# Kernel optimization log

Hardware: AMD Instinct MI355X
Metric: run time of the kernel (lower is better)

The kernel has to match this reference:

```python
import jax, jax.numpy as jnp
import numpy as np

B, N, D = 8, 2048, 8        # batch, nodes, input_dim == hidden_dim
E, DEC = 8, 128             # embedding_dim, decoder_dim


def _leaky(x, slope):
    return jnp.where(x >= 0, x, slope * x)


def _sage(x, attn, inv_deg, w, b):
    # adj transposed on dims (1,2) then left-matmul: new[b,i,d] = sum_j attn[b,j,i] x[b,j,d]
    new_x = jnp.einsum('bji,bjd->bid', attn, x)
    new_x = jnp.matmul(inv_deg, new_x)
    new_x = jnp.matmul(new_x, w)
    self_x = jnp.matmul(x, b)
    c = jnp.concatenate([new_x, self_x], axis=2)
    norm = jnp.sqrt(jnp.sum(c * c, axis=2, keepdims=True))
    return c / jnp.maximum(norm, 1e-12)  # F.normalize(p=2, dim=2)


def setup_inputs():
    key = jax.random.key(0)
    ks = jax.random.split(key, 12)
    x = jax.random.normal(ks[0], (B, N, D), jnp.float32)
    adj = jax.random.randint(ks[1], (B, N, N), 0, 2).astype(jnp.int32)
    deg = jnp.sum(adj.astype(jnp.float32), axis=2)
    inv_deg = jax.vmap(jnp.diag)(1.0 / (deg + 1.0))  # [B,N,N] diagonal
    g = np.sqrt(2.0)  # xavier-style scale stand-in
    W = jax.random.normal(ks[2], (D, D), jnp.float32) * (g / np.sqrt(2 * D))
    a = jax.random.normal(ks[3], (2 * D, 1), jnp.float32) * (g / np.sqrt(2 * D + 1))
    w1 = jax.random.normal(ks[4], (D, D), jnp.float32) * 0.3
    b1 = jax.random.normal(ks[5], (D, D), jnp.float32) * 0.3
    w2 = jax.random.normal(ks[6], (2 * D, D), jnp.float32) * 0.3
    b2 = jax.random.normal(ks[7], (2 * D, D), jnp.float32) * 0.3
    w3 = jax.random.normal(ks[8], (2 * D, E), jnp.float32) * 0.3
    b3 = jax.random.normal(ks[9], (2 * D, E), jnp.float32) * 0.3
    P1 = jax.random.normal(ks[10], (2 * E, DEC), jnp.float32) * 0.1
    P2 = jax.random.normal(ks[11], (DEC, DEC), jnp.float32) * 0.1
    return {"x": x, "adj": adj, "inv_deg": inv_deg, "W": W, "a": a,
            "w1": w1, "b1": b1, "w2": w2, "b2": b2, "w3": w3, "b3": b3,
            "P1": P1, "P2": P2}


def reference(x, adj, inv_deg, W, a, w1, b1, w2, b2, w3, b3, P1, P2):
    h = jnp.matmul(x, W)                          # [B,N,D]
    # e[b,i,j] = leaky(h[b,i].a1 + h[b,j].a2), equivalent to cat+matmul without O(N^2*2D) tensor
    f1 = jnp.matmul(h, a[:D, 0])                  # [B,N]
    f2 = jnp.matmul(h, a[D:, 0])                  # [B,N]
    e = _leaky(f1[:, :, None] + f2[:, None, :], 0.2)
    e = jnp.where(adj > 0, e, jnp.float32(-9e15))
    attn = jax.nn.softmax(e, axis=2)              # [B,N,N]
    out = _leaky(_sage(x, attn, inv_deg, w1, b1), 0.1)
    out = _leaky(_sage(out, attn, inv_deg, w2, b2), 0.1)
    out = _leaky(_sage(out, attn, inv_deg, w3, b3), 0.1)
    da = out[:, N - 2]                            # [B,2E]
    db = out[:, N - 1]
    ypred = jnp.einsum('bi,id,de,je,bj->b', da, P1, P2, P1, db)
    return ypred[:, None]
```

## Files before the change

kernel.cpp:

```cpp
#include <hip/hip_runtime.h>
#include <math.h>

constexpr int CB   = 8;
constexpr int CN   = 2048;
constexpr int CD   = 8;
constexpr int CDEC = 128;
constexpr int CBN  = CB * CN;
constexpr int NWRD = CN / 64;
constexpr int JSP  = 32;
constexpr int JLEN = CN / JSP;

__device__ __forceinline__ float msel(unsigned long long m, int lane, float p) {
  return ((m >> lane) & 1ull) ? p : 0.f;
}

__global__ void prep_k(const float* __restrict__ x,
                       const float* __restrict__ W, const float* __restrict__ a,
                       float4* __restrict__ pk, float4* __restrict__ qk) {
  int t = blockIdx.x * blockDim.x + threadIdx.x;
  if (t >= CBN) return;
  const float* xr = x + (size_t)t * CD;
  float h[CD];
#pragma unroll
  for (int d = 0; d < CD; ++d) {
    float s = 0.f;
#pragma unroll
    for (int k = 0; k < CD; ++k) s = fmaf(xr[k], W[k * CD + d], s);
    h[d] = s;
  }
  float s1 = 0.f, s2 = 0.f;
#pragma unroll
  for (int d = 0; d < CD; ++d) { s1 = fmaf(h[d], a[d], s1); s2 = fmaf(h[d], a[CD + d], s2); }
  pk[t] = make_float4(s1, expf(s1), expf(0.2f * s1), 0.f);
  qk[t] = make_float4(s2, expf(s2), expf(0.2f * s2), 0.f);
}

__global__ __launch_bounds__(256) void mask_k(const int* __restrict__ adj,
    float4* __restrict__ pk, const float4* __restrict__ qk,
    unsigned long long* __restrict__ maskT) {
  const int lane = threadIdx.x & 63;
  const int gw2 = blockIdx.x * 4 + (threadIdx.x >> 6);
  const int b = gw2 >> 9;
  const int jw = gw2 & 511;
  const int* ab = adj + (size_t)b * CN * CN;
  const float4* qb = qk + (size_t)b * CN;
  float f1[4];
#pragma unroll
  for (int r = 0; r < 4; ++r) f1[r] = pk[b * CN + jw + 512 * r].x;
  float A[4] = {0.f, 0.f, 0.f, 0.f}, C[4] = {0.f, 0.f, 0.f, 0.f};
  int deg[4] = {0, 0, 0, 0};
  for (int k = 0; k < NWRD; ++k) {
    int i = k * 64 + lane;
    float4 q = qb[i];
    unsigned long long m[4];
#pragma unroll
    for (int r = 0; r < 4; ++r) {
      bool bit = ab[(size_t)(jw + 512 * r) * CN + i] > 0;
      m[r] = __ballot(bit);
      bool cond = (f1[r] + q.x) >= 0.f;
      A[r] += (bit && cond) ? q.y : 0.f;
      C[r] += (bit && !cond) ? q.z : 0.f;
    }
    if (lane == 0) {
#pragma unroll
      for (int r = 0; r < 4; ++r) {
        maskT[((size_t)(b * NWRD + k)) * CN + jw + 512 * r] = m[r];
        deg[r] += __popcll(m[r]);
      }
    }
  }
#pragma unroll
  for (int r = 0; r < 4; ++r) {
#pragma unroll
    for (int off = 32; off; off >>= 1) {
      A[r] += __shfl_down(A[r], off);
      C[r] += __shfl_down(C[r], off);
    }
  }
  if (lane == 0) {
#pragma unroll
    for (int r = 0; r < 4; ++r) {
      int gr = b * CN + jw + 512 * r;
      float4 pj = pk[gr];
      float s = pj.y * A[r] + pj.z * C[r];
      float ga = (s > 0.f) ? pj.y / s : 0.f;
      float gb = (s > 0.f) ? pj.z / s : 0.f;
      float dv = 1.f / (float)(deg[r] + 1);
      pk[gr] = make_float4(pj.x, ga, gb, dv);
    }
  }
}

template <int DIN>
__global__ __launch_bounds__(256) void agg_k(const float* __restrict__ feat,
                      const unsigned long long* __restrict__ maskT,
                      const float4* __restrict__ pk, const float4* __restrict__ qk,
                      const float* __restrict__ wmat, float* __restrict__ part) {
  const int js = blockIdx.x, ic = blockIdx.y, b = blockIdx.z;
  const int t = threadIdx.x;
  const int w = __builtin_amdgcn_readfirstlane(t >> 6);
  const int lane = t & 63;
  const int i1 = ic * 512 + t, i2 = i1 + 256;
  const int gi1 = b * CN + i1, gi2 = b * CN + i2;
  float4 q1 = qk[gi1], q2 = qk[gi2];
  const unsigned long long* mc1 = maskT + ((size_t)(b * NWRD + ic * 8 + w)) * CN + js * JLEN;
  const unsigned long long* mc2 = maskT + ((size_t)(b * NWRD + ic * 8 + 4 + w)) * CN + js * JLEN;
  const float4* pb = pk + (size_t)b * CN + js * JLEN;
  const float* fb  = feat + ((size_t)b * CN + js * JLEN) * DIN;
  float acc1[DIN], acc2[DIN];
#pragma unroll
  for (int d = 0; d < DIN; ++d) { acc1[d] = 0.f; acc2[d] = 0.f; }
#pragma unroll 4
  for (int jj = 0; jj < JLEN; ++jj) {
    unsigned long long m1 = mc1[jj];
    unsigned long long m2 = mc2[jj];
    float4 pj = pb[jj];
    const float* fr = fb + jj * DIN;
    float wA = msel(m1, lane, fmaxf(pj.y * q1.y, pj.z * q1.z));
    float wB = msel(m2, lane, fmaxf(pj.y * q2.y, pj.z * q2.z));
#pragma unroll
    for (int d = 0; d < DIN; ++d) {
      acc1[d] = fmaf(wA, fr[d], acc1[d]);
      acc2[d] = fmaf(wB, fr[d], acc2[d]);
    }
  }
  float o1[8], o2[8];
#pragma unroll
  for (int o = 0; o < 8; ++o) {
    float s1 = 0.f, s2 = 0.f;
#pragma unroll
    for (int d = 0; d < DIN; ++d) {
      s1 = fmaf(acc1[d], wmat[d * 8 + o], s1);
      s2 = fmaf(acc2[d], wmat[d * 8 + o], s2);
    }
    o1[o] = s1;
    o2[o] = s2;
  }
  float4* p1 = (float4*)(part + ((size_t)js * CBN + gi1) * 8);
  float4* p2 = (float4*)(part + ((size_t)js * CBN + gi2) * 8);
  p1[0] = make_float4(o1[0], o1[1], o1[2], o1[3]);
  p1[1] = make_float4(o1[4], o1[5], o1[6], o1[7]);
  p2[0] = make_float4(o2[0], o2[1], o2[2], o2[3]);
  p2[1] = make_float4(o2[4], o2[5], o2[6], o2[7]);
}

__global__ void epi8_k(const float* __restrict__ part, const float* __restrict__ feat,
                       const float4* __restrict__ pk, const float* __restrict__ bmat,
                       float* __restrict__ out) {
  int t = blockIdx.x * blockDim.x + threadIdx.x;
  if (t >= CBN) return;
  float4 a0 = make_float4(0.f, 0.f, 0.f, 0.f), a1 = a0;
  for (int p_ = 0; p_ < JSP; ++p_) {
    const float4* pr = (const float4*)(part + ((size_t)p_ * CBN + t) * 8);
    float4 r0 = pr[0], r1 = pr[1];
    a0.x += r0.x; a0.y += r0.y; a0.z += r0.z; a0.w += r0.w;
    a1.x += r1.x; a1.y += r1.y; a1.z += r1.z; a1.w += r1.w;
  }
  float ag[8] = {a0.x, a0.y, a0.z, a0.w, a1.x, a1.y, a1.z, a1.w};
  float di = pk[t].w;
  const float* fr = feat + (size_t)t * 8;
  float c[16];
#pragma unroll
  for (int o = 0; o < 8; ++o) {
    float s2 = 0.f;
#pragma unroll
    for (int d = 0; d < 8; ++d) s2 = fmaf(fr[d], bmat[d * 8 + o], s2);
    c[o] = ag[o] * di;
    c[8 + o] = s2;
  }
  float nn = 0.f;
#pragma unroll
  for (int k = 0; k < 16; ++k) nn += c[k] * c[k];
  float inv = 1.f / fmaxf(sqrtf(nn), 1e-12f);
  float4* orow = (float4*)(out + (size_t)t * 16);
#pragma unroll
  for (int q = 0; q < 4; ++q) {
    float v0 = c[q*4+0]*inv, v1 = c[q*4+1]*inv, v2 = c[q*4+2]*inv, v3 = c[q*4+3]*inv;
    orow[q] = make_float4(v0 >= 0.f ? v0 : 0.1f*v0, v1 >= 0.f ? v1 : 0.1f*v1,
                          v2 >= 0.f ? v2 : 0.1f*v2, v3 >= 0.f ? v3 : 0.1f*v3);
  }
}

__global__ __launch_bounds__(256) void epi16f_k(
    const float* __restrict__ out1, const float* __restrict__ part2,
    const unsigned long long* __restrict__ maskT,
    const float4* __restrict__ pk, const float4* __restrict__ qk,
    const float* __restrict__ b2,
    float* __restrict__ gpart, float* __restrict__ self2) {
  __shared__ float redA[4][16], redB[4][16];
  const int t = threadIdx.x;
  const int lane = t & 63, wv = t >> 6;
  const int gr = blockIdx.x * 256 + t;
  const int b = blockIdx.x >> 3, blk8 = blockIdx.x & 7;
  const int j = gr - b * CN;
  const int ia = CN - 2, ib = CN - 1;
  float ag[8] = {0.f,0.f,0.f,0.f,0.f,0.f,0.f,0.f};
  for (int p = 0; p < JSP; ++p) {
    const float4* pr = (const float4*)(part2 + ((size_t)p * CBN + gr) * 8);
    float4 r0 = pr[0], r1 = pr[1];
    ag[0] += r0.x; ag[1] += r0.y; ag[2] += r0.z; ag[3] += r0.w;
    ag[4] += r1.x; ag[5] += r1.y; ag[6] += r1.z; ag[7] += r1.w;
  }
  float4 pj = pk[gr];
  const float4* o1p = (const float4*)(out1 + (size_t)gr * 16);
  float4 g0 = o1p[0], g1 = o1p[1], g2 = o1p[2], g3 = o1p[3];
  float of[16] = {g0.x,g0.y,g0.z,g0.w, g1.x,g1.y,g1.z,g1.w,
                  g2.x,g2.y,g2.z,g2.w, g3.x,g3.y,g3.z,g3.w};
  float c[16];
#pragma unroll
  for (int o = 0; o < 8; ++o) {
    float s2 = 0.f;
#pragma unroll
    for (int d = 0; d < 16; ++d) s2 = fmaf(of[d], b2[d * 8 + o], s2);
    c[o] = ag[o] * pj.w;
    c[8 + o] = s2;
  }
  float nn = 0.f;
#pragma unroll
  for (int k = 0; k < 16; ++k) nn += c[k] * c[k];
  float inv = 1.f / fmaxf(sqrtf(nn), 1e-12f);
  float ff[16];
#pragma unroll
  for (int k = 0; k < 16; ++k) {
    float v = c[k] * inv;
    ff[k] = (v >= 0.f) ? v : 0.1f * v;
  }
  if (j == ia || j == ib) {
    float* s = self2 + ((size_t)b * 2 + (j == ib ? 1 : 0)) * 16;
#pragma unroll
    for (int d = 0; d < 16; ++d) s[d] = ff[d];
  }
  unsigned long long m = maskT[((size_t)(b * NWRD + (NWRD - 1))) * CN + j];
  float4 qa = qk[b * CN + ia], qb = qk[b * CN + ib];
  float wA = ((m >> 62) & 1ull) ? fmaxf(pj.y * qa.y, pj.z * qa.z) : 0.f;
  float wB = (m >> 63) ? fmaxf(pj.y * qb.y, pj.z * qb.z) : 0.f;
  float accA[16], accB[16];
#pragma unroll
  for (int d = 0; d < 16; ++d) { accA[d] = wA * ff[d]; accB[d] = wB * ff[d]; }
#pragma unroll
  for (int d = 0; d < 16; ++d) {
#pragma unroll
    for (int off = 32; off; off >>= 1) {
      accA[d] += __shfl_down(accA[d], off);
      accB[d] += __shfl_down(accB[d], off);
    }
  }
  if (lane == 0) {
#pragma unroll
    for (int d = 0; d < 16; ++d) { redA[wv][d] = accA[d]; redB[wv][d] = accB[d]; }
  }
  __syncthreads();
  if (t < 32) {
    int row = t >> 4, k = t & 15;
    float s = row ? (redB[0][k] + redB[1][k] + redB[2][k] + redB[3][k])
                  : (redA[0][k] + redA[1][k] + redA[2][k] + redA[3][k]);
    gpart[(((size_t)b * 8 + blk8) * 2 + row) * 16 + k] = s;
  }
}

__global__ __launch_bounds__(CDEC) void dec_k(
    const float* __restrict__ gpart, const float* __restrict__ self2,
    const float4* __restrict__ pk,
    const float* __restrict__ w3, const float* __restrict__ b3,
    const float* __restrict__ P1, const float* __restrict__ P2,
    float* __restrict__ y) {
  __shared__ float agA[16], agB[16], cA[16], cB[16], daF[16], dbF[16];
  __shared__ float vsh[CDEC], red[CDEC];
  const int b = blockIdx.x;
  const int t = threadIdx.x;
  const int ia = CN - 2, ib = CN - 1;
  if (t < 32) {
    int row = t >> 4, k = t & 15;
    float s = 0.f;
#pragma unroll
    for (int blk = 0; blk < 8; ++blk)
      s += gpart[(((size_t)b * 8 + blk) * 2 + row) * 16 + k];
    float dv = pk[b * CN + (row ? ib : ia)].w;
    (row ? agB : agA)[k] = s * dv;
  }
  __syncthreads();
  if (t < 32) {
    int row = t >> 4, k = t & 15;
    const float* ag = row ? agB : agA;
    const float* self = self2 + ((size_t)b * 2 + row) * 16;
    float s = 0.f;
    if (k < 8) {
#pragma unroll
      for (int d = 0; d < 16; ++d) s = fmaf(ag[d], w3[d * 8 + k], s);
    } else {
#pragma unroll
      for (int d = 0; d < 16; ++d) s = fmaf(self[d], b3[d * 8 + (k - 8)], s);
    }
    (row ? cB : cA)[k] = s;
  }
  __syncthreads();
  if (t < 32) {
    int row = t >> 4, k = t & 15;
    const float* c = row ? cB : cA;
    float nn = 0.f;
#pragma unroll
    for (int q = 0; q < 16; ++q) nn += c[q] * c[q];
    float inv = 1.f / fmaxf(sqrtf(nn), 1e-12f);
    float v = c[k] * inv;
    (row ? dbF : daF)[k] = (v >= 0.f) ? v : 0.1f * v;
  }
  __syncthreads();
  float ue = 0.f, ve = 0.f;
#pragma unroll
  for (int i = 0; i < 16; ++i) {
    ue = fmaf(daF[i], P1[i * CDEC + t], ue);
    ve = fmaf(dbF[i], P1[i * CDEC + t], ve);
  }
  vsh[t] = ve;
  __syncthreads();
  float s = 0.f;
  for (int e2 = 0; e2 < CDEC; ++e2) s = fmaf(P2[t * CDEC + e2], vsh[e2], s);
  red[t] = s * ue;
  __syncthreads();
  for (int off = 64; off; off >>= 1) {
    if (t < off) red[t] += red[t + off];
    __syncthreads();
  }
  if (t == 0) y[b] = red[0];
}

extern "C" void kernel_launch(void* const* d_in, const int* in_sizes, int n_in,
                              void* d_out, int out_size, void* d_ws, size_t ws_size,
                              hipStream_t stream) {
  const float* x  = (const float*)d_in[0];
  const int*   adj = (const int*)d_in[1];
  const float* W  = (const float*)d_in[3];
  const float* a  = (const float*)d_in[4];
  const float* w1 = (const float*)d_in[5];
  const float* b1 = (const float*)d_in[6];
  const float* w2 = (const float*)d_in[7];
  const float* b2 = (const float*)d_in[8];
  const float* w3 = (const float*)d_in[9];
  const float* b3 = (const float*)d_in[10];
  const float* P1 = (const float*)d_in[11];
  const float* P2 = (const float*)d_in[12];
  float* y = (float*)d_out;

  char* base = (char*)d_ws;
  size_t off = 0;
  auto alloc = [&](size_t bytes) -> void* {
    void* r = base + off;
    off += (bytes + 255) & ~(size_t)255;
    return r;
  };
  float4* pk = (float4*)alloc(sizeof(float4) * CBN);
  float4* qk = (float4*)alloc(sizeof(float4) * CBN);
  unsigned long long* maskT =
      (unsigned long long*)alloc(sizeof(unsigned long long) * (size_t)CBN * NWRD);
  float* out1  = (float*)alloc(sizeof(float) * (size_t)CBN * 16);
  float* part  = (float*)alloc(sizeof(float) * (size_t)JSP * CBN * 8);
  float* gpart = (float*)alloc(sizeof(float) * CB * 8 * 2 * 16);
  float* self2 = (float*)alloc(sizeof(float) * CB * 2 * 16);

  hipLaunchKernelGGL(prep_k, dim3(CBN / 256), dim3(256), 0, stream, x, W, a, pk, qk);
  hipLaunchKernelGGL(mask_k, dim3(1024), dim3(256), 0, stream, adj, pk, qk, maskT);
  hipLaunchKernelGGL(agg_k<8>, dim3(JSP, 4, CB), dim3(256), 0, stream, x, maskT, pk, qk, w1, part);
  hipLaunchKernelGGL(epi8_k, dim3(CBN / 256), dim3(256), 0, stream, part, x, pk, b1, out1);
  hipLaunchKernelGGL(agg_k<16>, dim3(JSP, 4, CB), dim3(256), 0, stream, out1, maskT, pk, qk, w2, part);
  hipLaunchKernelGGL(epi16f_k, dim3(CBN / 256), dim3(256), 0, stream,
                     out1, part, maskT, pk, qk, b2, gpart, self2);
  hipLaunchKernelGGL(dec_k, dim3(CB), dim3(CDEC), 0, stream,
                     gpart, self2, pk, w3, b3, P1, P2, y);
}
```

Baseline: 109.0 us.

## Apply layer weight matrices before aggregation to shrink layer-2 feature width

Uses associativity, attn^T (x W) = (attn^T x) W, to project node features through w and b before the attention aggregation rather than after. The second aggregation then reads 8-wide pre-projected features instead of the 16-wide layer-1 output, which halves its feature loads and inner FMAs. The self-term projections are computed in the producer kernels. This adds extra per-node buffers and a small dense matmul in prep and epi8, and slightly changes floating-point summation order.

```diff
diff --git a/kernel.cpp b/kernel.cpp
--- a/kernel.cpp
+++ b/kernel.cpp
@@ -16,7 +16,9 @@
 
 __global__ void prep_k(const float* __restrict__ x,
                        const float* __restrict__ W, const float* __restrict__ a,
-                       float4* __restrict__ pk, float4* __restrict__ qk) {
+                       const float* __restrict__ w1, const float* __restrict__ b1,
+                       float4* __restrict__ pk, float4* __restrict__ qk,
+                       float* __restrict__ feat1w, float* __restrict__ selfb1) {
   int t = blockIdx.x * blockDim.x + threadIdx.x;
   if (t >= CBN) return;
   const float* xr = x + (size_t)t * CD;
@@ -33,6 +35,23 @@
   for (int d = 0; d < CD; ++d) { s1 = fmaf(h[d], a[d], s1); s2 = fmaf(h[d], a[CD + d], s2); }
   pk[t] = make_float4(s1, expf(s1), expf(0.2f * s1), 0.f);
   qk[t] = make_float4(s2, expf(s2), expf(0.2f * s2), 0.f);
+  float fw[8], fb[8];
+#pragma unroll
+  for (int o = 0; o < 8; ++o) {
+    float sw = 0.f, sb = 0.f;
+#pragma unroll
+    for (int d = 0; d < CD; ++d) {
+      sw = fmaf(xr[d], w1[d * 8 + o], sw);
+      sb = fmaf(xr[d], b1[d * 8 + o], sb);
+    }
+    fw[o] = sw; fb[o] = sb;
+  }
+  float4* f4 = (float4*)(feat1w + (size_t)t * 8);
+  f4[0] = make_float4(fw[0], fw[1], fw[2], fw[3]);
+  f4[1] = make_float4(fw[4], fw[5], fw[6], fw[7]);
+  float4* s4 = (float4*)(selfb1 + (size_t)t * 8);
+  s4[0] = make_float4(fb[0], fb[1], fb[2], fb[3]);
+  s4[1] = make_float4(fb[4], fb[5], fb[6], fb[7]);
 }
 
 __global__ __launch_bounds__(256) void mask_k(const int* __restrict__ adj,
@@ -91,11 +110,10 @@
   }
 }
 
-template <int DIN>
-__global__ __launch_bounds__(256) void agg_k(const float* __restrict__ feat,
+__global__ __launch_bounds__(256) void aggf_k(const float* __restrict__ feat,
                       const unsigned long long* __restrict__ maskT,
                       const float4* __restrict__ pk, const float4* __restrict__ qk,
-                      const float* __restrict__ wmat, float* __restrict__ part) {
+                      float* __restrict__ part) {
   const int js = blockIdx.x, ic = blockIdx.y, b = blockIdx.z;
   const int t = threadIdx.x;
   const int w = __builtin_amdgcn_readfirstlane(t >> 6);
@@ -106,47 +124,36 @@
   const unsigned long long* mc1 = maskT + ((size_t)(b * NWRD + ic * 8 + w)) * CN + js * JLEN;
   const unsigned long long* mc2 = maskT + ((size_t)(b * NWRD + ic * 8 + 4 + w)) * CN + js * JLEN;
   const float4* pb = pk + (size_t)b * CN + js * JLEN;
-  const float* fb  = feat + ((size_t)b * CN + js * JLEN) * DIN;
-  float acc1[DIN], acc2[DIN];
-#pragma unroll
-  for (int d = 0; d < DIN; ++d) { acc1[d] = 0.f; acc2[d] = 0.f; }
+  const float* fb  = feat + ((size_t)b * CN + js * JLEN) * 8;
+  float acc1[8], acc2[8];
+#pragma unroll
+  for (int d = 0; d < 8; ++d) { acc1[d] = 0.f; acc2[d] = 0.f; }
 #pragma unroll 4
   for (int jj = 0; jj < JLEN; ++jj) {
     unsigned long long m1 = mc1[jj];
     unsigned long long m2 = mc2[jj];
     float4 pj = pb[jj];
-    const float* fr = fb + jj * DIN;
+    const float* fr = fb + jj * 8;
     float wA = msel(m1, lane, fmaxf(pj.y * q1.y, pj.z * q1.z));
     float wB = msel(m2, lane, fmaxf(pj.y * q2.y, pj.z * q2.z));
 #pragma unroll
-    for (int d = 0; d < DIN; ++d) {
+    for (int d = 0; d < 8; ++d) {
       acc1[d] = fmaf(wA, fr[d], acc1[d]);
       acc2[d] = fmaf(wB, fr[d], acc2[d]);
     }
   }
-  float o1[8], o2[8];
-#pragma unroll
-  for (int o = 0; o < 8; ++o) {
-    float s1 = 0.f, s2 = 0.f;
-#pragma unroll
-    for (int d = 0; d < DIN; ++d) {
-      s1 = fmaf(acc1[d], wmat[d * 8 + o], s1);
-      s2 = fmaf(acc2[d], wmat[d * 8 + o], s2);
-    }
-    o1[o] = s1;
-    o2[o] = s2;
-  }
   float4* p1 = (float4*)(part + ((size_t)js * CBN + gi1) * 8);
   float4* p2 = (float4*)(part + ((size_t)js * CBN + gi2) * 8);
-  p1[0] = make_float4(o1[0], o1[1], o1[2], o1[3]);
-  p1[1] = make_float4(o1[4], o1[5], o1[6], o1[7]);
-  p2[0] = make_float4(o2[0], o2[1], o2[2], o2[3]);
-  p2[1] = make_float4(o2[4], o2[5], o2[6], o2[7]);
-}
-
-__global__ void epi8_k(const float* __restrict__ part, const float* __restrict__ feat,
-                       const float4* __restrict__ pk, const float* __restrict__ bmat,
-                       float* __restrict__ out) {
+  p1[0] = make_float4(acc1[0], acc1[1], acc1[2], acc1[3]);
+  p1[1] = make_float4(acc1[4], acc1[5], acc1[6], acc1[7]);
+  p2[0] = make_float4(acc2[0], acc2[1], acc2[2], acc2[3]);
+  p2[1] = make_float4(acc2[4], acc2[5], acc2[6], acc2[7]);
+}
+
+__global__ void epi8_k(const float* __restrict__ part, const float* __restrict__ selfb1,
+                       const float4* __restrict__ pk,
+                       const float* __restrict__ w2, const float* __restrict__ b2,
+                       float* __restrict__ feat2w, float* __restrict__ selfb2) {
   int t = blockIdx.x * blockDim.x + threadIdx.x;
   if (t >= CBN) return;
   float4 a0 = make_float4(0.f, 0.f, 0.f, 0.f), a1 = a0;
@@ -156,36 +163,45 @@
     a0.x += r0.x; a0.y += r0.y; a0.z += r0.z; a0.w += r0.w;
     a1.x += r1.x; a1.y += r1.y; a1.z += r1.z; a1.w += r1.w;
   }
-  float ag[8] = {a0.x, a0.y, a0.z, a0.w, a1.x, a1.y, a1.z, a1.w};
   float di = pk[t].w;
-  const float* fr = feat + (size_t)t * 8;
-  float c[16];
-#pragma unroll
-  for (int o = 0; o < 8; ++o) {
-    float s2 = 0.f;
-#pragma unroll
-    for (int d = 0; d < 8; ++d) s2 = fmaf(fr[d], bmat[d * 8 + o], s2);
-    c[o] = ag[o] * di;
-    c[8 + o] = s2;
-  }
+  const float4* sb = (const float4*)(selfb1 + (size_t)t * 8);
+  float4 s0 = sb[0], s1 = sb[1];
+  float c[16] = {a0.x * di, a0.y * di, a0.z * di, a0.w * di,
+                 a1.x * di, a1.y * di, a1.z * di, a1.w * di,
+                 s0.x, s0.y, s0.z, s0.w, s1.x, s1.y, s1.z, s1.w};
   float nn = 0.f;
 #pragma unroll
   for (int k = 0; k < 16; ++k) nn += c[k] * c[k];
   float inv = 1.f / fmaxf(sqrtf(nn), 1e-12f);
-  float4* orow = (float4*)(out + (size_t)t * 16);
-#pragma unroll
-  for (int q = 0; q < 4; ++q) {
-    float v0 = c[q*4+0]*inv, v1 = c[q*4+1]*inv, v2 = c[q*4+2]*inv, v3 = c[q*4+3]*inv;
-    orow[q] = make_float4(v0 >= 0.f ? v0 : 0.1f*v0, v1 >= 0.f ? v1 : 0.1f*v1,
-                          v2 >= 0.f ? v2 : 0.1f*v2, v3 >= 0.f ? v3 : 0.1f*v3);
-  }
+  float ff[16];
+#pragma unroll
+  for (int k = 0; k < 16; ++k) {
+    float v = c[k] * inv;
+    ff[k] = (v >= 0.f) ? v : 0.1f * v;
+  }
+  float fw[8], fb[8];
+#pragma unroll
+  for (int o = 0; o < 8; ++o) {
+    float sw = 0.f, sb2_ = 0.f;
+#pragma unroll
+    for (int d = 0; d < 16; ++d) {
+      sw = fmaf(ff[d], w2[d * 8 + o], sw);
+      sb2_ = fmaf(ff[d], b2[d * 8 + o], sb2_);
+    }
+    fw[o] = sw; fb[o] = sb2_;
+  }
+  float4* f4 = (float4*)(feat2w + (size_t)t * 8);
+  f4[0] = make_float4(fw[0], fw[1], fw[2], fw[3]);
+  f4[1] = make_float4(fw[4], fw[5], fw[6], fw[7]);
+  float4* s4 = (float4*)(selfb2 + (size_t)t * 8);
+  s4[0] = make_float4(fb[0], fb[1], fb[2], fb[3]);
+  s4[1] = make_float4(fb[4], fb[5], fb[6], fb[7]);
 }
 
 __global__ __launch_bounds__(256) void epi16f_k(
-    const float* __restrict__ out1, const float* __restrict__ part2,
+    const float* __restrict__ part2, const float* __restrict__ selfb2,
     const unsigned long long* __restrict__ maskT,
     const float4* __restrict__ pk, const float4* __restrict__ qk,
-    const float* __restrict__ b2,
     float* __restrict__ gpart, float* __restrict__ self2) {
   __shared__ float redA[4][16], redB[4][16];
   const int t = threadIdx.x;
@@ -194,27 +210,19 @@
   const int b = blockIdx.x >> 3, blk8 = blockIdx.x & 7;
   const int j = gr - b * CN;
   const int ia = CN - 2, ib = CN - 1;
-  float ag[8] = {0.f,0.f,0.f,0.f,0.f,0.f,0.f,0.f};
+  float4 a0 = make_float4(0.f, 0.f, 0.f, 0.f), a1 = a0;
   for (int p = 0; p < JSP; ++p) {
     const float4* pr = (const float4*)(part2 + ((size_t)p * CBN + gr) * 8);
     float4 r0 = pr[0], r1 = pr[1];
-    ag[0] += r0.x; ag[1] += r0.y; ag[2] += r0.z; ag[3] += r0.w;
-    ag[4] += r1.x; ag[5] += r1.y; ag[6] += r1.z; ag[7] += r1.w;
+    a0.x += r0.x; a0.y += r0.y; a0.z += r0.z; a0.w += r0.w;
+    a1.x += r1.x; a1.y += r1.y; a1.z += r1.z; a1.w += r1.w;
   }
   float4 pj = pk[gr];
-  const float4* o1p = (const float4*)(out1 + (size_t)gr * 16);
-  float4 g0 = o1p[0], g1 = o1p[1], g2 = o1p[2], g3 = o1p[3];
-  float of[16] = {g0.x,g0.y,g0.z,g0.w, g1.x,g1.y,g1.z,g1.w,
-                  g2.x,g2.y,g2.z,g2.w, g3.x,g3.y,g3.z,g3.w};
-  float c[16];
-#pragma unroll
-  for (int o = 0; o < 8; ++o) {
-    float s2 = 0.f;
-#pragma unroll
-    for (int d = 0; d < 16; ++d) s2 = fmaf(of[d], b2[d * 8 + o], s2);
-    c[o] = ag[o] * pj.w;
-    c[8 + o] = s2;
-  }
+  const float4* sb = (const float4*)(selfb2 + (size_t)gr * 8);
+  float4 s0 = sb[0], s1 = sb[1];
+  float c[16] = {a0.x * pj.w, a0.y * pj.w, a0.z * pj.w, a0.w * pj.w,
+                 a1.x * pj.w, a1.y * pj.w, a1.z * pj.w, a1.w * pj.w,
+                 s0.x, s0.y, s0.z, s0.w, s1.x, s1.y, s1.z, s1.w};
   float nn = 0.f;
 #pragma unroll
   for (int k = 0; k < 16; ++k) nn += c[k] * c[k];
@@ -352,18 +360,23 @@
   float4* qk = (float4*)alloc(sizeof(float4) * CBN);
   unsigned long long* maskT =
       (unsigned long long*)alloc(sizeof(unsigned long long) * (size_t)CBN * NWRD);
-  float* out1  = (float*)alloc(sizeof(float) * (size_t)CBN * 16);
-  float* part  = (float*)alloc(sizeof(float) * (size_t)JSP * CBN * 8);
-  float* gpart = (float*)alloc(sizeof(float) * CB * 8 * 2 * 16);
-  float* self2 = (float*)alloc(sizeof(float) * CB * 2 * 16);
-
-  hipLaunchKernelGGL(prep_k, dim3(CBN / 256), dim3(256), 0, stream, x, W, a, pk, qk);
+  float* feat1w = (float*)alloc(sizeof(float) * (size_t)CBN * 8);
+  float* selfb1 = (float*)alloc(sizeof(float) * (size_t)CBN * 8);
+  float* feat2w = (float*)alloc(sizeof(float) * (size_t)CBN * 8);
+  float* selfb2 = (float*)alloc(sizeof(float) * (size_t)CBN * 8);
+  float* part   = (float*)alloc(sizeof(float) * (size_t)JSP * CBN * 8);
+  float* gpart  = (float*)alloc(sizeof(float) * CB * 8 * 2 * 16);
+  float* self2  = (float*)alloc(sizeof(float) * CB * 2 * 16);
+
+  hipLaunchKernelGGL(prep_k, dim3(CBN / 256), dim3(256), 0, stream,
+                     x, W, a, w1, b1, pk, qk, feat1w, selfb1);
   hipLaunchKernelGGL(mask_k, dim3(1024), dim3(256), 0, stream, adj, pk, qk, maskT);
-  hipLaunchKernelGGL(agg_k<8>, dim3(JSP, 4, CB), dim3(256), 0, stream, x, maskT, pk, qk, w1, part);
-  hipLaunchKernelGGL(epi8_k, dim3(CBN / 256), dim3(256), 0, stream, part, x, pk, b1, out1);
-  hipLaunchKernelGGL(agg_k<16>, dim3(JSP, 4, CB), dim3(256), 0, stream, out1, maskT, pk, qk, w2, part);
+  hipLaunchKernelGGL(aggf_k, dim3(JSP, 4, CB), dim3(256), 0, stream, feat1w, maskT, pk, qk, part);
+  hipLaunchKernelGGL(epi8_k, dim3(CBN / 256), dim3(256), 0, stream,
+                     part, selfb1, pk, w2, b2, feat2w, selfb2);
+  hipLaunchKernelGGL(aggf_k, dim3(JSP, 4, CB), dim3(256), 0, stream, feat2w, maskT, pk, qk, part);
   hipLaunchKernelGGL(epi16f_k, dim3(CBN / 256), dim3(256), 0, stream,
-                     out1, part, maskT, pk, qk, b2, gpart, self2);
+                     part, selfb2, maskT, pk, qk, gpart, self2);
   hipLaunchKernelGGL(dec_k, dim3(CB), dim3(CDEC), 0, stream,
                      gpart, self2, pk, w3, b3, P1, P2, y);
 }
```

Result: faster. 102.3 us (-6.2%).
